# Kernel tuning notes

Measured on AMD Instinct MI355X. Metric: run time of the kernel, lower is better.

The kernel has to match this reference:

```python
import jax, jax.numpy as jnp
import numpy as np

B, N, HID, H, D = 16, 512, 1024, 16, 64
T_HOP, T_EDGE = 32, 64
SCALE = D ** -0.5


def _forward(x, query_hop_emb, query_edge_emb, key_hop_emb, key_edge_emb,
             value_hop_emb, value_edge_emb, hop, edge_matrix,
             Wq, bq, Wk, bk, Wv, bv, Wo, bo):
    b, n, _ = x.shape
    # projections -> [B,H,N,D]
    q = (x @ Wq.T + bq).reshape(b, n, H, D).transpose(0, 2, 1, 3)
    k = (x @ Wk.T + bk).reshape(b, n, H, D).transpose(0, 2, 1, 3)
    v = (x @ Wv.T + bv).reshape(b, n, H, D).transpose(0, 2, 1, 3)

    # embeddings -> [T,H,D]
    qhe = query_hop_emb.reshape(T_HOP, H, D)
    qee = query_edge_emb.reshape(T_EDGE, H, D)
    khe = key_hop_emb.reshape(T_HOP, H, D)
    kee = key_edge_emb.reshape(T_EDGE, H, D)
    vhe = value_hop_emb.reshape(T_HOP, H, D)
    vee = value_edge_emb.reshape(T_EDGE, H, D)

    hop_b = jnp.broadcast_to(hop[:, None, :, :], (b, H, n, n))          # [B,H,N,N]
    edge_b = jnp.broadcast_to(edge_matrix[:, None, :, :], (b, H, n, n))

    # q/k vs hop/edge type scores: [B,H,N,T], then gather along T by hop/edge index
    q_hop = jnp.take_along_axis(jnp.einsum('bhnd,thd->bhnt', q, qhe), hop_b, axis=3)
    q_edge = jnp.take_along_axis(jnp.einsum('bhnd,thd->bhnt', q, qee), edge_b, axis=3)
    k_hop = jnp.take_along_axis(jnp.einsum('bhnd,thd->bhnt', k, khe), hop_b, axis=3)
    k_edge = jnp.take_along_axis(jnp.einsum('bhnd,thd->bhnt', k, kee), edge_b, axis=3)

    spatial_bias = q_hop + k_hop
    edge_bias = q_edge + k_edge

    att = jnp.einsum('bhid,bhjd->bhij', q, k)
    logits = (att + (spatial_bias + edge_bias)) * SCALE  # scale applied after bias, as in source
    att = jax.nn.softmax(logits, axis=3)

    # scatter-add attention weights into hop/edge type buckets: [B,H,N,T]
    bi = jnp.arange(b)[:, None, None, None]
    hi = jnp.arange(H)[None, :, None, None]
    ni = jnp.arange(n)[None, None, :, None]
    vha = jnp.zeros((b, H, n, T_HOP), att.dtype).at[bi, hi, ni, hop_b].add(att)
    vea = jnp.zeros((b, H, n, T_EDGE), att.dtype).at[bi, hi, ni, edge_b].add(att)

    x1 = jnp.einsum('bhij,bhjd->bhid', att, v)
    x2 = jnp.einsum('bhnt,thd->bhnd', vha, vhe)
    x3 = jnp.einsum('bhnt,thd->bhnd', vea, vee)

    out = (x1 + (x2 + x3)).transpose(0, 2, 1, 3).reshape(b, n, H * D)
    return out @ Wo.T + bo


def setup_inputs() -> dict:
    key = jax.random.key(0)
    ks = jax.random.split(key, 20)
    s = 0.02
    return {
        'x': jax.random.normal(ks[0], (B, N, HID), jnp.float32),
        'query_hop_emb': jax.random.normal(ks[1], (T_HOP, HID), jnp.float32) * s,
        'query_edge_emb': jax.random.normal(ks[2], (T_EDGE, HID), jnp.float32) * s,
        'key_hop_emb': jax.random.normal(ks[3], (T_HOP, HID), jnp.float32) * s,
        'key_edge_emb': jax.random.normal(ks[4], (T_EDGE, HID), jnp.float32) * s,
        'value_hop_emb': jax.random.normal(ks[5], (T_HOP, HID), jnp.float32) * s,
        'value_edge_emb': jax.random.normal(ks[6], (T_EDGE, HID), jnp.float32) * s,
        'hop': jax.random.randint(ks[7], (B, N, N), 0, T_HOP, jnp.int32),
        'edge_matrix': jax.random.randint(ks[8], (B, N, N), 0, T_EDGE, jnp.int32),
        'Wq': jax.random.normal(ks[9], (HID, HID), jnp.float32) * s,
        'bq': jnp.zeros((HID,), jnp.float32),
        'Wk': jax.random.normal(ks[10], (HID, HID), jnp.float32) * s,
        'bk': jnp.zeros((HID,), jnp.float32),
        'Wv': jax.random.normal(ks[11], (HID, HID), jnp.float32) * s,
        'bv': jnp.zeros((HID,), jnp.float32),
        'Wo': jax.random.normal(ks[12], (HID, HID), jnp.float32) * s,
        'bo': jnp.zeros((HID,), jnp.float32),
    }


def reference(x, query_hop_emb, query_edge_emb, key_hop_emb, key_edge_emb,
              value_hop_emb, value_edge_emb, hop, edge_matrix,
              Wq, bq, Wk, bk, Wv, bv, Wo, bo):
    return _forward(x, query_hop_emb, query_edge_emb, key_hop_emb, key_edge_emb,
                    value_hop_emb, value_edge_emb, hop, edge_matrix,
                    Wq, bq, Wk, bk, Wv, bv, Wo, bo)
```

## Files before the change

kernel.cpp:

```cpp
#include <hip/hip_runtime.h>


#define SCALE 0.125f

typedef __attribute__((ext_vector_type(8))) short bf16x8;
typedef __attribute__((ext_vector_type(4))) float f32x4;

__device__ __forceinline__ ushort f2bf(float x) {
    unsigned u = __float_as_uint(x);
    return (ushort)((u + 0x7FFF + ((u >> 16) & 1)) >> 16);
}
__device__ __forceinline__ float bf2f(ushort h) {
    return __uint_as_float(((unsigned)h) << 16);
}

__device__ __forceinline__ void stage16(const ushort* g, ushort* l) {
    __builtin_amdgcn_global_load_lds(
        (const __attribute__((address_space(1))) unsigned int*)g,
        (__attribute__((address_space(3))) unsigned int*)l, 16, 0, 0);
}

__global__ __launch_bounds__(256) void split_bf16(
    const float* __restrict__ in, ushort* __restrict__ oh,
    ushort* __restrict__ ol, int n)
{
    const int stride = gridDim.x * 256 * 4;
    for (int i = (blockIdx.x * 256 + threadIdx.x) * 4; i < n; i += stride) {
        float4 v = *(const float4*)&in[i];
        ushort4 h, l;
        h.x = f2bf(v.x); l.x = f2bf(v.x - bf2f(h.x));
        h.y = f2bf(v.y); l.y = f2bf(v.y - bf2f(h.y));
        h.z = f2bf(v.z); l.z = f2bf(v.z - bf2f(h.z));
        h.w = f2bf(v.w); l.w = f2bf(v.w - bf2f(h.w));
        *(ushort4*)&oh[i] = h;
        *(ushort4*)&ol[i] = l;
    }
}

__global__ __launch_bounds__(256) void gemm_mfma(
    const ushort* __restrict__ Ah, const ushort* __restrict__ Al,
    const ushort* __restrict__ Bh, const ushort* __restrict__ Bl,
    const float* __restrict__ bias, float* __restrict__ Cf,
    ushort* __restrict__ Ch, ushort* __restrict__ Cl, int layout)
{
    __shared__ ushort sAh[4096];
    __shared__ ushort sAl[4096];
    __shared__ ushort sBh[2048];
    __shared__ ushort sBl[2048];

    const int tid = threadIdx.x;
    const int m0 = blockIdx.x * 128, n0 = blockIdx.y * 64;
    const int l = tid & 63, w = tid >> 6;
    const int wr = w >> 1, wc = w & 1;
    const int koff = l >> 4, r16 = l & 15;

    f32x4 acc[4][2] = {};

    const int sa0 = tid, sa1 = tid + 256;
    const int ar0 = sa0 & 127, ak0 = sa0 >> 7;
    const int ar1 = sa1 & 127, ak1 = sa1 >> 7;
    const int bn = tid & 63, bk = tid >> 6;

    const ushort* gAh0 = Ah + (size_t)(m0 + ar0) * 1024 + ak0 * 8;
    const ushort* gAh1 = Ah + (size_t)(m0 + ar1) * 1024 + ak1 * 8;
    const ushort* gAl0 = Al + (size_t)(m0 + ar0) * 1024 + ak0 * 8;
    const ushort* gAl1 = Al + (size_t)(m0 + ar1) * 1024 + ak1 * 8;
    const ushort* gBh0 = Bh + (size_t)(n0 + bn) * 1024 + bk * 8;
    const ushort* gBl0 = Bl + (size_t)(n0 + bn) * 1024 + bk * 8;

    for (int kt = 0; kt < 32; ++kt) {
        const int k0 = kt * 32;
        __syncthreads();
        stage16(gAh0 + k0, &sAh[sa0 * 8]);
        stage16(gAh1 + k0, &sAh[sa1 * 8]);
        stage16(gAl0 + k0, &sAl[sa0 * 8]);
        stage16(gAl1 + k0, &sAl[sa1 * 8]);
        stage16(gBh0 + k0, &sBh[tid * 8]);
        stage16(gBl0 + k0, &sBl[tid * 8]);
        __syncthreads();

        bf16x8 fah[4], fal[4], fbh[2], fbl[2];
#pragma unroll
        for (int mi = 0; mi < 4; ++mi) {
            const int off = (koff * 128 + wr * 64 + mi * 16 + r16) * 8;
            fah[mi] = *(const bf16x8*)&sAh[off];
            fal[mi] = *(const bf16x8*)&sAl[off];
        }
#pragma unroll
        for (int ni = 0; ni < 2; ++ni) {
            const int off = (koff * 64 + wc * 32 + ni * 16 + r16) * 8;
            fbh[ni] = *(const bf16x8*)&sBh[off];
            fbl[ni] = *(const bf16x8*)&sBl[off];
        }
#pragma unroll
        for (int mi = 0; mi < 4; ++mi)
#pragma unroll
            for (int ni = 0; ni < 2; ++ni) {
                acc[mi][ni] = __builtin_amdgcn_mfma_f32_16x16x32_bf16(
                    fah[mi], fbh[ni], acc[mi][ni], 0, 0, 0);
                acc[mi][ni] = __builtin_amdgcn_mfma_f32_16x16x32_bf16(
                    fah[mi], fbl[ni], acc[mi][ni], 0, 0, 0);
                acc[mi][ni] = __builtin_amdgcn_mfma_f32_16x16x32_bf16(
                    fal[mi], fbh[ni], acc[mi][ni], 0, 0, 0);
            }
    }

#pragma unroll
    for (int mi = 0; mi < 4; ++mi) {
        const int rowb = m0 + wr * 64 + mi * 16 + (l >> 4) * 4;
#pragma unroll
        for (int ni = 0; ni < 2; ++ni) {
            const int col = n0 + wc * 32 + ni * 16 + (l & 15);
            const float bb = bias[col];
            float v[4];
#pragma unroll
            for (int r = 0; r < 4; ++r) v[r] = acc[mi][ni][r] + bb;
            if (layout == 0) {
#pragma unroll
                for (int r = 0; r < 4; ++r)
                    Cf[(size_t)(rowb + r) * 1024 + col] = v[r];
            } else if (layout == 1) {
                const int b16_ = rowb >> 9, i2 = rowb & 511;
                const int hh = col >> 6, dd = col & 63;
                const size_t base = ((size_t)(b16_ * 16 + hh) * 512 + i2) * 64 + dd;
#pragma unroll
                for (int r = 0; r < 4; ++r) {
                    ushort hv_ = f2bf(v[r]);
                    Ch[base + (size_t)r * 64] = hv_;
                    Cl[base + (size_t)r * 64] = f2bf(v[r] - bf2f(hv_));
                }
            } else {
                const int b16_ = rowb >> 9, i2 = rowb & 511;
                const int hh = col >> 6, dd = col & 63;
                ushort4 pk;
                pk.x = f2bf(v[0]); pk.y = f2bf(v[1]);
                pk.z = f2bf(v[2]); pk.w = f2bf(v[3]);
                *(ushort4*)&Ch[((size_t)(b16_ * 16 + hh) * 64 + dd) * 512 + i2] = pk;
            }
        }
    }
}

__global__ __launch_bounds__(256) void type_scores(
    const ushort* __restrict__ Qh, const ushort* __restrict__ Ql,
    const ushort* __restrict__ Kh, const ushort* __restrict__ Kl,
    const float* __restrict__ qhe, const float* __restrict__ qee,
    const float* __restrict__ khe, const float* __restrict__ kee,
    ushort* __restrict__ Shop, ushort* __restrict__ Sedge)
{
    __shared__ float qs[64][65];
    __shared__ float ks[64][65];
    const int tid = threadIdx.x;
    const int i0 = (blockIdx.x & 7) * 64;
    const int bh = blockIdx.x >> 3;
    const int h = bh & 15;
    {
        const int r = tid >> 2, c16 = (tid & 3) << 4;
        const size_t off = ((size_t)bh * 512 + i0 + r) * 64 + c16;
        ushort tqh[16], tql[16], tkh[16], tkl[16];
        *(uint4*)&tqh[0] = *(const uint4*)&Qh[off];
        *(uint4*)&tqh[8] = *(const uint4*)&Qh[off + 8];
        *(uint4*)&tql[0] = *(const uint4*)&Ql[off];
        *(uint4*)&tql[8] = *(const uint4*)&Ql[off + 8];
        *(uint4*)&tkh[0] = *(const uint4*)&Kh[off];
        *(uint4*)&tkh[8] = *(const uint4*)&Kh[off + 8];
        *(uint4*)&tkl[0] = *(const uint4*)&Kl[off];
        *(uint4*)&tkl[8] = *(const uint4*)&Kl[off + 8];
#pragma unroll
        for (int u = 0; u < 16; ++u) {
            qs[r][c16 + u] = bf2f(tqh[u]) + bf2f(tql[u]);
            ks[r][c16 + u] = bf2f(tkh[u]) + bf2f(tkl[u]);
        }
    }
    __syncthreads();
    const int i = tid & 63;
    const int tq = tid >> 6;
    for (int tt = 0; tt < 24; ++tt) {
        int t96 = tq * 24 + tt;
        const float *eq, *ek;
        ushort* outp;
        if (t96 < 32) {
            eq = qhe + t96 * 1024 + h * 64;
            ek = khe + t96 * 1024 + h * 64;
            outp = &Shop[((size_t)bh * 512 + i0 + i) * 32 + t96];
        } else {
            int t = t96 - 32;
            eq = qee + t * 1024 + h * 64;
            ek = kee + t * 1024 + h * 64;
            outp = &Sedge[((size_t)bh * 512 + i0 + i) * 64 + t];
        }
        float s0 = 0.f, s1 = 0.f, s2 = 0.f, s3 = 0.f;
#pragma unroll 4
        for (int d = 0; d < 64; d += 4) {
            s0 += qs[i][d + 0] * eq[d + 0] + ks[i][d + 0] * ek[d + 0];
            s1 += qs[i][d + 1] * eq[d + 1] + ks[i][d + 1] * ek[d + 1];
            s2 += qs[i][d + 2] * eq[d + 2] + ks[i][d + 2] * ek[d + 2];
            s3 += qs[i][d + 3] * eq[d + 3] + ks[i][d + 3] * ek[d + 3];
        }
        *outp = f2bf((s0 + s1) + (s2 + s3));
    }
}

__global__ __launch_bounds__(256) void attn_mfma(
    const ushort* __restrict__ Qh, const ushort* __restrict__ Ql,
    const ushort* __restrict__ Kh, const ushort* __restrict__ Kl,
    const ushort* __restrict__ Vtb,
    const ushort* __restrict__ ShopB, const ushort* __restrict__ SedgeB,
    const int* __restrict__ hop, const int* __restrict__ edge,
    const float* __restrict__ vhe, const float* __restrict__ vee,
    float* __restrict__ Y)
{
    __shared__ ushort sKh[4096];
    __shared__ ushort sKl[4096];
    __shared__ ushort sVt[4096];
    __shared__ ushort sP[4096];
    __shared__ ushort sShop[2048];
    __shared__ ushort sSedge[4096];
    __shared__ float vha[2112];
    __shared__ float vea[4160];

    const int tid = threadIdx.x;
    const int bid = blockIdx.x;
    const int swz = (bid & 7) * 256 + (bid >> 3);
    const int it = swz & 7, h = (swz >> 3) & 15, b = swz >> 7;
    const int bh = b * 16 + h;
    const int i0 = it * 64;

    const int l = tid & 63, w = tid >> 6;
    const int l15 = l & 15, lhi = l >> 4;
    const int xorv = (l15 & 7) << 4;

    {
        const ushort* sh = ShopB + ((size_t)bh * 512 + i0) * 32 + tid * 8;
        *(uint4*)&sShop[tid * 8] = *(const uint4*)sh;
        const ushort* se = SedgeB + ((size_t)bh * 512 + i0) * 64 + tid * 16;
        *(uint4*)&sSedge[tid * 16] = *(const uint4*)se;
        *(uint4*)&sSedge[tid * 16 + 8] = *(const uint4*)(se + 8);
    }
    for (int i = tid; i < 2112; i += 256) vha[i] = 0.f;
    for (int i = tid; i < 4160; i += 256) vea[i] = 0.f;

    bf16x8 qfh[2], qfl[2];
    {
        const size_t q0 = ((size_t)bh * 512 + i0 + w * 16 + l15) * 64 + lhi * 8;
        qfh[0] = *(const bf16x8*)&Qh[q0];
        qfh[1] = *(const bf16x8*)&Qh[q0 + 32];
        qfl[0] = *(const bf16x8*)&Ql[q0];
        qfl[1] = *(const bf16x8*)&Ql[q0 + 32];
    }

    f32x4 accO[4] = {};
    float m_run[4] = {-1e30f, -1e30f, -1e30f, -1e30f};
    float l_run[4] = {0.f, 0.f, 0.f, 0.f};

    const int sj = tid >> 3;
    const int sc = ((tid & 7) ^ (sj & 7)) * 8;
    const size_t kb = (size_t)bh * 32768;

    const char* sKhB = (const char*)sKh;
    const char* sKlB = (const char*)sKl;
    const char* sVtB = (const char*)sVt;
    char* sPB = (char*)sP;
    const int wpb = w * 2048;

    for (int t = 0; t < 8; ++t) {
        const int j0 = t * 64;
        __syncthreads();
        stage16(&Kh[kb + (size_t)(j0 + sj) * 64 + sc], &sKh[tid * 8]);
        stage16(&Kh[kb + (size_t)(j0 + sj + 32) * 64 + sc], &sKh[(tid + 256) * 8]);
        stage16(&Kl[kb + (size_t)(j0 + sj) * 64 + sc], &sKl[tid * 8]);
        stage16(&Kl[kb + (size_t)(j0 + sj + 32) * 64 + sc], &sKl[(tid + 256) * 8]);
        stage16(&Vtb[kb + (size_t)sj * 512 + j0 + sc], &sVt[tid * 8]);
        stage16(&Vtb[kb + (size_t)(sj + 32) * 512 + j0 + sc], &sVt[(tid + 256) * 8]);
        __syncthreads();

        int hv[16], ev[16];
        {
            const size_t rb = ((size_t)b * 512 + i0 + w * 16 + lhi * 4) * 512 + j0 + l15;
            const int* hp = hop + rb;
            const int* ep = edge + rb;
#pragma unroll
            for (int r = 0; r < 4; ++r)
#pragma unroll
                for (int cf = 0; cf < 4; ++cf) {
                    hv[cf * 4 + r] = hp[r * 512 + cf * 16];
                    ev[cf * 4 + r] = ep[r * 512 + cf * 16];
                }
        }

        f32x4 S[4] = {};
#pragma unroll
        for (int ks = 0; ks < 2; ++ks) {
            const int rb2 = (ks * 64 + lhi * 16) ^ xorv;
#pragma unroll
            for (int cf = 0; cf < 4; ++cf) {
                const int jrow = (cf * 16 + l15) * 128;
                bf16x8 kh_ = *(const bf16x8*)(sKhB + jrow + rb2);
                bf16x8 kl_ = *(const bf16x8*)(sKlB + jrow + rb2);
                S[cf] = __builtin_amdgcn_mfma_f32_16x16x32_bf16(qfh[ks], kh_, S[cf], 0, 0, 0);
                S[cf] = __builtin_amdgcn_mfma_f32_16x16x32_bf16(qfh[ks], kl_, S[cf], 0, 0, 0);
                S[cf] = __builtin_amdgcn_mfma_f32_16x16x32_bf16(qfl[ks], kh_, S[cf], 0, 0, 0);
            }
        }

        float val[16];
#pragma unroll
        for (int cf = 0; cf < 4; ++cf)
#pragma unroll
            for (int r = 0; r < 4; ++r) {
                const int rg = w * 16 + lhi * 4 + r;
                val[cf * 4 + r] = (S[cf][r] + bf2f(sShop[rg * 32 + hv[cf * 4 + r]])
                                   + bf2f(sSedge[rg * 64 + ev[cf * 4 + r]])) * SCALE;
            }
        float tmax[4];
#pragma unroll
        for (int r = 0; r < 4; ++r) {
            float tm = fmaxf(fmaxf(val[r], val[4 + r]), fmaxf(val[8 + r], val[12 + r]));
            tm = fmaxf(tm, __shfl_xor(tm, 1));
            tm = fmaxf(tm, __shfl_xor(tm, 2));
            tm = fmaxf(tm, __shfl_xor(tm, 4));
            tm = fmaxf(tm, __shfl_xor(tm, 8));
            tmax[r] = tm;
        }
        const bool need = (tmax[0] > m_run[0] + 10.f) || (tmax[1] > m_run[1] + 10.f) ||
                          (tmax[2] > m_run[2] + 10.f) || (tmax[3] > m_run[3] + 10.f);
        if (__any(need)) {
#pragma unroll
            for (int r = 0; r < 4; ++r) {
                const float mn = fmaxf(m_run[r], tmax[r]);
                const float al = __expf(m_run[r] - mn);
                m_run[r] = mn;
                l_run[r] *= al;
                accO[0][r] *= al; accO[1][r] *= al;
                accO[2][r] *= al; accO[3][r] *= al;
                const int rg = w * 16 + lhi * 4 + r;
                vha[rg * 33 + l15] *= al;
                vha[rg * 33 + 16 + l15] *= al;
                vea[rg * 65 + l15] *= al;
                vea[rg * 65 + 16 + l15] *= al;
                vea[rg * 65 + 32 + l15] *= al;
                vea[rg * 65 + 48 + l15] *= al;
            }
            asm volatile("" ::: "memory");
        }
        float p[16];
        float ps[4] = {0.f, 0.f, 0.f, 0.f};
#pragma unroll
        for (int cf = 0; cf < 4; ++cf)
#pragma unroll
            for (int r = 0; r < 4; ++r) {
                const float pe = __expf(val[cf * 4 + r] - m_run[r]);
                p[cf * 4 + r] = pe;
                ps[r] += pe;
            }
#pragma unroll
        for (int r = 0; r < 4; ++r) {
            float s_ = ps[r];
            s_ += __shfl_xor(s_, 1);
            s_ += __shfl_xor(s_, 2);
            s_ += __shfl_xor(s_, 4);
            s_ += __shfl_xor(s_, 8);
            l_run[r] += s_;
        }
#pragma unroll
        for (int cf = 0; cf < 4; ++cf)
#pragma unroll
            for (int r = 0; r < 4; ++r) {
                const int rg = w * 16 + lhi * 4 + r;
                atomicAdd(&vha[rg * 33 + hv[cf * 4 + r]], p[cf * 4 + r]);
                atomicAdd(&vea[rg * 65 + ev[cf * 4 + r]], p[cf * 4 + r]);
                const int rl = lhi * 4 + r;
                *(ushort*)(sPB + wpb + rl * 128 +
                           ((cf * 32 + l15 * 2) ^ ((rl & 7) << 4))) = f2bf(p[cf * 4 + r]);
            }
        asm volatile("" ::: "memory");

#pragma unroll
        for (int ks = 0; ks < 2; ++ks) {
            const int rb2 = (ks * 64 + lhi * 16) ^ xorv;
            bf16x8 pa = *(const bf16x8*)(sPB + wpb + l15 * 128 + rb2);
#pragma unroll
            for (int cf = 0; cf < 4; ++cf) {
                bf16x8 vb = *(const bf16x8*)(sVtB + (cf * 16 + l15) * 128 + rb2);
                accO[cf] = __builtin_amdgcn_mfma_f32_16x16x32_bf16(pa, vb, accO[cf], 0, 0, 0);
            }
        }
    }
    asm volatile("" ::: "memory");

    float inv[4];
#pragma unroll
    for (int r = 0; r < 4; ++r) inv[r] = 1.0f / l_run[r];
    float o[16];
#pragma unroll
    for (int cf = 0; cf < 4; ++cf)
#pragma unroll
        for (int r = 0; r < 4; ++r) o[cf * 4 + r] = accO[cf][r] * inv[r];

    const int rgb = w * 16 + lhi * 4;
    for (int tt = 0; tt < 32; ++tt) {
        float wn[4];
#pragma unroll
        for (int r = 0; r < 4; ++r) wn[r] = vha[(rgb + r) * 33 + tt] * inv[r];
        const float* g = vhe + (size_t)tt * 1024 + h * 64 + l15;
#pragma unroll
        for (int cf = 0; cf < 4; ++cf) {
            const float gv = g[cf * 16];
#pragma unroll
            for (int r = 0; r < 4; ++r) o[cf * 4 + r] += wn[r] * gv;
        }
    }
    for (int tt = 0; tt < 64; ++tt) {
        float wn[4];
#pragma unroll
        for (int r = 0; r < 4; ++r) wn[r] = vea[(rgb + r) * 65 + tt] * inv[r];
        const float* g = vee + (size_t)tt * 1024 + h * 64 + l15;
#pragma unroll
        for (int cf = 0; cf < 4; ++cf) {
            const float gv = g[cf * 16];
#pragma unroll
            for (int r = 0; r < 4; ++r) o[cf * 4 + r] += wn[r] * gv;
        }
    }
#pragma unroll
    for (int r = 0; r < 4; ++r) {
        float* yp = Y + ((size_t)b * 512 + i0 + rgb + r) * 1024 + h * 64 + l15;
#pragma unroll
        for (int cf = 0; cf < 4; ++cf) yp[cf * 16] = o[cf * 4 + r];
    }
}

extern "C" void kernel_launch(void* const* d_in, const int* in_sizes, int n_in,
                              void* d_out, int out_size, void* d_ws, size_t ws_size,
                              hipStream_t stream)
{
    (void)in_sizes; (void)n_in; (void)out_size; (void)ws_size;
    const float* x   = (const float*)d_in[0];
    const float* qhe = (const float*)d_in[1];
    const float* qee = (const float*)d_in[2];
    const float* khe = (const float*)d_in[3];
    const float* kee = (const float*)d_in[4];
    const float* vhe = (const float*)d_in[5];
    const float* vee = (const float*)d_in[6];
    const int*   hop = (const int*)d_in[7];
    const int*   edg = (const int*)d_in[8];
    const float* Wq = (const float*)d_in[9];  const float* bq = (const float*)d_in[10];
    const float* Wk = (const float*)d_in[11]; const float* bk = (const float*)d_in[12];
    const float* Wv = (const float*)d_in[13]; const float* bv = (const float*)d_in[14];
    const float* Wo = (const float*)d_in[15]; const float* bo = (const float*)d_in[16];

    ushort* Qh    = (ushort*)d_ws;
    ushort* Ql    = Qh + 8388608;
    ushort* Kh    = Ql + 8388608;
    ushort* Kl    = Kh + 8388608;
    ushort* VtB   = Kl + 8388608;
    ushort* ShopB = VtB + 8388608;
    ushort* SedgeB= ShopB + 4194304;
    float*  Yb    = (float*)(SedgeB + 8388608);
    ushort* xh    = (ushort*)(Yb + 8388608);
    ushort* xl    = xh + 8388608;
    ushort* wh    = xl + 8388608;
    ushort* wl    = wh + 1048576;

    const dim3 gG(64, 16);

    split_bf16<<<2048, 256, 0, stream>>>(x, xh, xl, 8388608);
    split_bf16<<<512, 256, 0, stream>>>(Wq, wh, wl, 1048576);
    gemm_mfma<<<gG, 256, 0, stream>>>(xh, xl, wh, wl, bq, nullptr, Qh, Ql, 1);
    split_bf16<<<512, 256, 0, stream>>>(Wk, wh, wl, 1048576);
    gemm_mfma<<<gG, 256, 0, stream>>>(xh, xl, wh, wl, bk, nullptr, Kh, Kl, 1);
    split_bf16<<<512, 256, 0, stream>>>(Wv, wh, wl, 1048576);
    gemm_mfma<<<gG, 256, 0, stream>>>(xh, xl, wh, wl, bv, nullptr, VtB, nullptr, 2);

    type_scores<<<2048, 256, 0, stream>>>(Qh, Ql, Kh, Kl, qhe, qee, khe, kee,
                                          ShopB, SedgeB);
    attn_mfma<<<2048, 256, 0, stream>>>(Qh, Ql, Kh, Kl, VtB, ShopB, SedgeB,
                                        hop, edg, vhe, vee, Yb);

    split_bf16<<<2048, 256, 0, stream>>>(Yb, xh, xl, 8388608);
    split_bf16<<<512, 256, 0, stream>>>(Wo, wh, wl, 1048576);
    gemm_mfma<<<gG, 256, 0, stream>>>(xh, xl, wh, wl, bo, (float*)d_out,
                                      nullptr, nullptr, 0);
}
```

Baseline: 1.543 ms.

## Pack hop/edge indices into 16-bit pairs and stage them through LDS

Adds a pre-pass kernel that packs the int32 hop and edge index matrices into one ushort per element. The attention kernel then stages those packed indices into shared memory with async global-to-LDS loads, instead of issuing 32 scattered int32 global loads per thread per tile. The intent is to cut the index traffic in the attention kernel by about 4x and replace strided uncoalesced loads with coalesced 16-byte transfers. In exchange there is an extra kernel pass over hop/edge each call, more LDS per block (which may lower occupancy), some register reuse of S in place of separate val/p arrays, and partial unrolling of the epilogue embedding loops.

```diff
diff --git a/kernel.cpp b/kernel.cpp
--- a/kernel.cpp
+++ b/kernel.cpp
@@ -18,6 +18,23 @@
     __builtin_amdgcn_global_load_lds(
         (const __attribute__((address_space(1))) unsigned int*)g,
         (__attribute__((address_space(3))) unsigned int*)l, 16, 0, 0);
+}
+
+__global__ __launch_bounds__(256) void pack_he(
+    const int* __restrict__ hop, const int* __restrict__ edge,
+    ushort* __restrict__ he, int n)
+{
+    const int stride = gridDim.x * 256 * 4;
+    for (int i = (blockIdx.x * 256 + threadIdx.x) * 4; i < n; i += stride) {
+        int4 hv = *(const int4*)&hop[i];
+        int4 ev = *(const int4*)&edge[i];
+        ushort4 o;
+        o.x = (ushort)(hv.x | (ev.x << 8));
+        o.y = (ushort)(hv.y | (ev.y << 8));
+        o.z = (ushort)(hv.z | (ev.z << 8));
+        o.w = (ushort)(hv.w | (ev.w << 8));
+        *(ushort4*)&he[i] = o;
+    }
 }
 
 __global__ __launch_bounds__(256) void split_bf16(
@@ -206,7 +223,7 @@
     const ushort* __restrict__ Kh, const ushort* __restrict__ Kl,
     const ushort* __restrict__ Vtb,
     const ushort* __restrict__ ShopB, const ushort* __restrict__ SedgeB,
-    const int* __restrict__ hop, const int* __restrict__ edge,
+    const ushort* __restrict__ heP,
     const float* __restrict__ vhe, const float* __restrict__ vee,
     float* __restrict__ Y)
 {
@@ -214,6 +231,7 @@
     __shared__ ushort sKl[4096];
     __shared__ ushort sVt[4096];
     __shared__ ushort sP[4096];
+    __shared__ ushort sHE[4096];
     __shared__ ushort sShop[2048];
     __shared__ ushort sSedge[4096];
     __shared__ float vha[2112];
@@ -256,6 +274,7 @@
     const int sj = tid >> 3;
     const int sc = ((tid & 7) ^ (sj & 7)) * 8;
     const size_t kb = (size_t)bh * 32768;
+    const ushort* heb = heP + ((size_t)b * 512 + i0 + w * 16 + (l >> 3)) * 512 + (l & 7) * 8;
 
     const char* sKhB = (const char*)sKh;
     const char* sKlB = (const char*)sKl;
@@ -272,21 +291,9 @@
         stage16(&Kl[kb + (size_t)(j0 + sj + 32) * 64 + sc], &sKl[(tid + 256) * 8]);
         stage16(&Vtb[kb + (size_t)sj * 512 + j0 + sc], &sVt[tid * 8]);
         stage16(&Vtb[kb + (size_t)(sj + 32) * 512 + j0 + sc], &sVt[(tid + 256) * 8]);
+        stage16(heb + j0, &sHE[w * 1024 + l * 8]);
+        stage16(heb + j0 + 8 * 512, &sHE[w * 1024 + 512 + l * 8]);
         __syncthreads();
-
-        int hv[16], ev[16];
-        {
-            const size_t rb = ((size_t)b * 512 + i0 + w * 16 + lhi * 4) * 512 + j0 + l15;
-            const int* hp = hop + rb;
-            const int* ep = edge + rb;
-#pragma unroll
-            for (int r = 0; r < 4; ++r)
-#pragma unroll
-                for (int cf = 0; cf < 4; ++cf) {
-                    hv[cf * 4 + r] = hp[r * 512 + cf * 16];
-                    ev[cf * 4 + r] = ep[r * 512 + cf * 16];
-                }
-        }
 
         f32x4 S[4] = {};
 #pragma unroll
@@ -303,19 +310,20 @@
             }
         }
 
-        float val[16];
 #pragma unroll
         for (int cf = 0; cf < 4; ++cf)
 #pragma unroll
             for (int r = 0; r < 4; ++r) {
                 const int rg = w * 16 + lhi * 4 + r;
-                val[cf * 4 + r] = (S[cf][r] + bf2f(sShop[rg * 32 + hv[cf * 4 + r]])
-                                   + bf2f(sSedge[rg * 64 + ev[cf * 4 + r]])) * SCALE;
-            }
+                const unsigned he = sHE[rg * 64 + cf * 16 + l15];
+                S[cf][r] = (S[cf][r] + bf2f(sShop[rg * 32 + (he & 255u)])
+                            + bf2f(sSedge[rg * 64 + (he >> 8)])) * SCALE;
+            }
+
         float tmax[4];
 #pragma unroll
         for (int r = 0; r < 4; ++r) {
-            float tm = fmaxf(fmaxf(val[r], val[4 + r]), fmaxf(val[8 + r], val[12 + r]));
+            float tm = fmaxf(fmaxf(S[0][r], S[1][r]), fmaxf(S[2][r], S[3][r]));
             tm = fmaxf(tm, __shfl_xor(tm, 1));
             tm = fmaxf(tm, __shfl_xor(tm, 2));
             tm = fmaxf(tm, __shfl_xor(tm, 4));
@@ -343,14 +351,14 @@
             }
             asm volatile("" ::: "memory");
         }
-        float p[16];
+
         float ps[4] = {0.f, 0.f, 0.f, 0.f};
 #pragma unroll
         for (int cf = 0; cf < 4; ++cf)
 #pragma unroll
             for (int r = 0; r < 4; ++r) {
-                const float pe = __expf(val[cf * 4 + r] - m_run[r]);
-                p[cf * 4 + r] = pe;
+                const float pe = __expf(S[cf][r] - m_run[r]);
+                S[cf][r] = pe;
                 ps[r] += pe;
             }
 #pragma unroll
@@ -362,16 +370,19 @@
             s_ += __shfl_xor(s_, 8);
             l_run[r] += s_;
         }
+
 #pragma unroll
         for (int cf = 0; cf < 4; ++cf)
 #pragma unroll
             for (int r = 0; r < 4; ++r) {
                 const int rg = w * 16 + lhi * 4 + r;
-                atomicAdd(&vha[rg * 33 + hv[cf * 4 + r]], p[cf * 4 + r]);
-                atomicAdd(&vea[rg * 65 + ev[cf * 4 + r]], p[cf * 4 + r]);
+                const unsigned he = sHE[rg * 64 + cf * 16 + l15];
+                const float pv = S[cf][r];
+                atomicAdd(&vha[rg * 33 + (he & 255u)], pv);
+                atomicAdd(&vea[rg * 65 + (he >> 8)], pv);
                 const int rl = lhi * 4 + r;
                 *(ushort*)(sPB + wpb + rl * 128 +
-                           ((cf * 32 + l15 * 2) ^ ((rl & 7) << 4))) = f2bf(p[cf * 4 + r]);
+                           ((cf * 32 + l15 * 2) ^ ((rl & 7) << 4))) = f2bf(pv);
             }
         asm volatile("" ::: "memory");
 
@@ -398,6 +409,7 @@
         for (int r = 0; r < 4; ++r) o[cf * 4 + r] = accO[cf][r] * inv[r];
 
     const int rgb = w * 16 + lhi * 4;
+#pragma unroll 4
     for (int tt = 0; tt < 32; ++tt) {
         float wn[4];
 #pragma unroll
@@ -410,6 +422,7 @@
             for (int r = 0; r < 4; ++r) o[cf * 4 + r] += wn[r] * gv;
         }
     }
+#pragma unroll 4
     for (int tt = 0; tt < 64; ++tt) {
         float wn[4];
 #pragma unroll
@@ -456,7 +469,8 @@
     ushort* VtB   = Kl + 8388608;
     ushort* ShopB = VtB + 8388608;
     ushort* SedgeB= ShopB + 4194304;
-    float*  Yb    = (float*)(SedgeB + 8388608);
+    ushort* heB   = SedgeB + 8388608;
+    float*  Yb    = (float*)(heB + 4194304);
     ushort* xh    = (ushort*)(Yb + 8388608);
     ushort* xl    = xh + 8388608;
     ushort* wh    = xl + 8388608;
@@ -464,6 +478,7 @@
 
     const dim3 gG(64, 16);
 
+    pack_he<<<2048, 256, 0, stream>>>(hop, edg, heB, 4194304);
     split_bf16<<<2048, 256, 0, stream>>>(x, xh, xl, 8388608);
     split_bf16<<<512, 256, 0, stream>>>(Wq, wh, wl, 1048576);
     gemm_mfma<<<gG, 256, 0, stream>>>(xh, xl, wh, wl, bq, nullptr, Qh, Ql, 1);
@@ -475,7 +490,7 @@
     type_scores<<<2048, 256, 0, stream>>>(Qh, Ql, Kh, Kl, qhe, qee, khe, kee,
                                           ShopB, SedgeB);
     attn_mfma<<<2048, 256, 0, stream>>>(Qh, Ql, Kh, Kl, VtB, ShopB, SedgeB,
-                                        hop, edg, vhe, vee, Yb);
+                                        heB, vhe, vee, Yb);
 
     split_bf16<<<2048, 256, 0, stream>>>(Yb, xh, xl, 8388608);
     split_bf16<<<512, 256, 0, stream>>>(Wo, wh, wl, 1048576);
```

Measured after the change: 1.555 ms. No clear change (+0.8%).
